# Optimization experiments

Hardware: AMD Instinct MI355X
Metric: run time of the kernel (lower is better)

## Reference

```python
import jax, jax.numpy as jnp
import numpy as np

EPS = 1e-5

def _gcn_norm(edge_index, num_nodes):
    # add self loops (improved=False -> fill value 1.0), symmetric normalization
    src = jnp.concatenate([edge_index[0], jnp.arange(num_nodes)])
    dst = jnp.concatenate([edge_index[1], jnp.arange(num_nodes)])
    w = jnp.ones(src.shape[0], dtype=jnp.float32)
    deg = jax.ops.segment_sum(w, dst, num_segments=num_nodes)
    dinv = jnp.where(deg > 0, 1.0 / jnp.sqrt(deg), 0.0)
    norm = dinv[src] * dinv[dst]  # [E+N]
    return src, dst, norm

def _gcn_conv(x, W, src, dst, norm, num_nodes):
    h = x @ W                      # [N, out]
    msg = h[src] * norm[:, None]   # gather + scale, [E+N, out]
    return jax.ops.segment_sum(msg, dst, num_segments=num_nodes)

def _bn_relu(x, gamma, beta):
    # BatchNorm1d in training mode: biased batch stats over the node dim
    m = x.mean(axis=0)
    v = x.var(axis=0)
    return jax.nn.relu((x - m) * jax.lax.rsqrt(v + EPS) * gamma + beta)

def setup_inputs() -> dict:
    key = jax.random.key(0)
    ks = jax.random.split(key, 12)
    N, E, D_IN, H, D_OUT, DEPTH = 100000, 1600000, 3, 128, 1, 9
    x = jax.random.normal(ks[0], (N, D_IN), dtype=jnp.float32)
    edge_index = jax.random.randint(ks[1], (2, E), 0, N, dtype=jnp.int64)
    s = 1.0 / np.sqrt(H)
    W0 = jax.random.normal(ks[2], (D_IN, H), jnp.float32) / np.sqrt(D_IN)
    Ws1 = jax.random.normal(ks[3], (DEPTH, H, H), jnp.float32) * s
    g1 = jnp.ones((DEPTH + 1, H), jnp.float32)
    b1 = jnp.zeros((DEPTH + 1, H), jnp.float32)
    Ws2 = jax.random.normal(ks[4], (DEPTH - 1, H, H), jnp.float32) * s
    g2 = jnp.ones((DEPTH - 1, H), jnp.float32)
    b2 = jnp.zeros((DEPTH - 1, H), jnp.float32)
    Wout = jax.random.normal(ks[5], (H, D_OUT), jnp.float32) * s
    return {"x": x, "edge_index": edge_index, "W0": W0, "Ws1": Ws1, "g1": g1,
            "b1": b1, "Ws2": Ws2, "g2": g2, "b2": b2, "Wout": Wout}

def reference(x, edge_index, W0, Ws1, g1, b1, Ws2, g2, b2, Wout):
    N = x.shape[0]
    depth = Ws1.shape[0]  # 9
    src, dst, norm = _gcn_norm(edge_index, N)
    # conv1[0]
    h = _bn_relu(_gcn_conv(x, W0, src, dst, norm, N), g1[0], b1[0])
    xs = [h]
    for i in range(1, depth + 1):
        h = _bn_relu(_gcn_conv(h, Ws1[i - 1], src, dst, norm, N), g1[i], b1[i])
        if i < depth:
            xs.append(h)
    for i in range(depth):
        j = depth - i - 1
        h = h + xs[j]
        if i < depth - 1:
            h = _bn_relu(_gcn_conv(h, Ws2[i], src, dst, norm, N), g2[i], b2[i])
        else:
            h = jax.nn.sigmoid(_gcn_conv(h, Wout, src, dst, norm, N))
    return h
```

## Files before the change

kernel.cpp:

```cpp
#include <hip/hip_runtime.h>
#include <hip/hip_bf16.h>

#define EPSV 1e-5f
#define NSTRIPE 16

typedef unsigned int uint;
typedef unsigned short ushort;
typedef __attribute__((ext_vector_type(8))) __bf16 bf16x8;
typedef __attribute__((ext_vector_type(4))) float f32x4;

static __device__ __forceinline__ float bf2f(ushort u) {
    return __uint_as_float(((uint)u) << 16);
}
static __device__ __forceinline__ ushort f2bf(float f) {
    __hip_bfloat16 h = __float2bfloat16(f);
    return __builtin_bit_cast(ushort, h);
}


static __device__ __forceinline__ float e4m3_dec(unsigned char b) {
    int s = b >> 7, E = (b >> 3) & 15, m = b & 7;
    float v = (E == 0) ? (float)m * 0.001953125f
                       : (float)(8 + m) * 0.125f * exp2f((float)(E - 7));
    return s ? -v : v;
}
static __device__ __forceinline__ unsigned char e4m3_enc(float f) {
    unsigned su = (__float_as_uint(f) >> 24) & 0x80u;
    float a = fabsf(f);
    if (!(a < 448.f)) return (unsigned char)(su | 0x7E);
    if (a < 0.015625f) {
        int m = (int)rintf(a * 512.f);
        return (unsigned char)(su | (m >= 8 ? 0x08 : m));
    }
    int e;
    frexpf(a, &e);
    int E = e - 1 + 7;
    float mant = a * exp2f((float)(1 - e)) - 1.0f;
    int mi = (int)rintf(mant * 8.f);
    if (mi >= 8) { mi = 0; E++; }
    if (E >= 16) return (unsigned char)(su | 0x7E);
    if (E == 15 && mi == 7) mi = 6;
    return (unsigned char)(su | (E << 3) | mi);
}


template <typename T> struct IOV;
template <> struct IOV<float> {
    static __device__ __forceinline__ float2 ld2(const float* p) { return *(const float2*)p; }
    static __device__ __forceinline__ void st2(float* p, float a, float b) {
        *(float2*)p = make_float2(a, b);
    }
    static __device__ __forceinline__ void ld8(const float* p, float* v) {
        float4 a = ((const float4*)p)[0], b = ((const float4*)p)[1];
        v[0] = a.x; v[1] = a.y; v[2] = a.z; v[3] = a.w;
        v[4] = b.x; v[5] = b.y; v[6] = b.z; v[7] = b.w;
    }
    static __device__ __forceinline__ void st8(float* p, const float* v) {
        ((float4*)p)[0] = make_float4(v[0], v[1], v[2], v[3]);
        ((float4*)p)[1] = make_float4(v[4], v[5], v[6], v[7]);
    }
};
template <> struct IOV<ushort> {
    static __device__ __forceinline__ float2 ld2(const ushort* p) {
        uint u = *(const uint*)p;
        return make_float2(bf2f((ushort)u), bf2f((ushort)(u >> 16)));
    }
    static __device__ __forceinline__ void st2(ushort* p, float a, float b) {
        *(uint*)p = (uint)f2bf(a) | ((uint)f2bf(b) << 16);
    }
    static __device__ __forceinline__ void ld8(const ushort* p, float* v) {
        uint4 u = *(const uint4*)p;
        v[0] = bf2f((ushort)u.x); v[1] = bf2f((ushort)(u.x >> 16));
        v[2] = bf2f((ushort)u.y); v[3] = bf2f((ushort)(u.y >> 16));
        v[4] = bf2f((ushort)u.z); v[5] = bf2f((ushort)(u.z >> 16));
        v[6] = bf2f((ushort)u.w); v[7] = bf2f((ushort)(u.w >> 16));
    }
    static __device__ __forceinline__ void st8(ushort* p, const float* v) {
        uint4 u;
        u.x = (uint)f2bf(v[0]) | ((uint)f2bf(v[1]) << 16);
        u.y = (uint)f2bf(v[2]) | ((uint)f2bf(v[3]) << 16);
        u.z = (uint)f2bf(v[4]) | ((uint)f2bf(v[5]) << 16);
        u.w = (uint)f2bf(v[6]) | ((uint)f2bf(v[7]) << 16);
        *(uint4*)p = u;
    }
};
template <> struct IOV<unsigned char> {
    static __device__ __forceinline__ float2 ld2(const unsigned char* p) {
        ushort u = *(const ushort*)p;
        return make_float2(e4m3_dec((unsigned char)u), e4m3_dec((unsigned char)(u >> 8)));
    }
    static __device__ __forceinline__ void st2(unsigned char* p, float a, float b) {
        *(ushort*)p = (ushort)e4m3_enc(a) | ((ushort)e4m3_enc(b) << 8);
    }
    static __device__ __forceinline__ void ld8(const unsigned char* p, float* v) {
        uint2 u = *(const uint2*)p;
#pragma unroll
        for (int j = 0; j < 4; j++) v[j] = e4m3_dec((unsigned char)(u.x >> (8 * j)));
#pragma unroll
        for (int j = 0; j < 4; j++) v[4 + j] = e4m3_dec((unsigned char)(u.y >> (8 * j)));
    }
    static __device__ __forceinline__ void st8(unsigned char* p, const float* v) {
        uint2 u = {0, 0};
#pragma unroll
        for (int j = 0; j < 4; j++) u.x |= (uint)e4m3_enc(v[j]) << (8 * j);
#pragma unroll
        for (int j = 0; j < 4; j++) u.y |= (uint)e4m3_enc(v[4 + j]) << (8 * j);
        *(uint2*)p = u;
    }
};


__global__ void k_count(const int* __restrict__ dst, int* __restrict__ cnt, int E) {
    int e = blockIdx.x * blockDim.x + threadIdx.x;
    if (e < E) atomicAdd(&cnt[dst[e]], 1);
}

__global__ void k_scan1(const int* __restrict__ cnt, int* __restrict__ bsum, int N) {
    __shared__ int s[256];
    int i = blockIdx.x * 256 + threadIdx.x;
    s[threadIdx.x] = (i < N) ? ((cnt[i] + 15) & ~15) : 0;
    __syncthreads();
    for (int o = 128; o > 0; o >>= 1) {
        if (threadIdx.x < o) s[threadIdx.x] += s[threadIdx.x + o];
        __syncthreads();
    }
    if (threadIdx.x == 0) bsum[blockIdx.x] = s[0];
}

__global__ void k_scan2(int* __restrict__ bsum, int B) {
    __shared__ int s[1024];
    int t = threadIdx.x;
    int orig = (t < B) ? bsum[t] : 0;
    s[t] = orig;
    __syncthreads();
    for (int o = 1; o < 1024; o <<= 1) {
        int v = (t >= o) ? s[t - o] : 0;
        __syncthreads();
        s[t] += v;
        __syncthreads();
    }
    if (t < B) bsum[t] = s[t] - orig;
}

__global__ void k_scan3(const int* __restrict__ cnt, const int* __restrict__ bsum,
                        int* __restrict__ roff, int* __restrict__ cursor,
                        float* __restrict__ dinv, int N) {
    __shared__ int s[256];
    int i = blockIdx.x * 256 + threadIdx.x;
    int v = (i < N) ? cnt[i] : 0;
    int pv = (v + 15) & ~15;
    s[threadIdx.x] = pv;
    __syncthreads();
    for (int o = 1; o < 256; o <<= 1) {
        int u = (threadIdx.x >= o) ? s[threadIdx.x - o] : 0;
        __syncthreads();
        s[threadIdx.x] += u;
        __syncthreads();
    }
    if (i < N) {
        int off = bsum[blockIdx.x] + s[threadIdx.x] - pv;
        roff[i] = off;
        cursor[i] = off;
        dinv[i] = rsqrtf((float)(v + 1));
        if (i == N - 1) roff[N] = off + pv;
    }
}

__global__ void k_scatter(const int* __restrict__ src, const int* __restrict__ dst,
                          const float* __restrict__ dinv, int* __restrict__ cursor,
                          int2* __restrict__ ev, int E) {
    int e = blockIdx.x * blockDim.x + threadIdx.x;
    if (e < E) {
        int s = src[e], d = dst[e];
        int p = atomicAdd(&cursor[d], 1);
        int2 pk;
        pk.x = s;
        pk.y = __float_as_int(dinv[s] * dinv[d]);
        ev[p] = pk;
    }
}

__global__ void k_pad(const int* __restrict__ cursor, const int* __restrict__ roff,
                      int2* __restrict__ ev, int N) {
    int i = blockIdx.x * blockDim.x + threadIdx.x;
    if (i >= N) return;
    int p = cursor[i], e = roff[i + 1];
    int2 pk;
    pk.x = i;
    pk.y = 0;
    for (; p < e; p++) ev[p] = pk;
}

__global__ void k_prepw(const float* __restrict__ Ws1, const float* __restrict__ Ws2,
                        ushort* __restrict__ whi, ushort* __restrict__ wlo) {
    int idx = blockIdx.x * blockDim.x + threadIdx.x;
    if (idx >= 17 * 16384) return;
    int L = idx >> 14, r = idx & 16383;
    int f = r >> 9, e = r & 511, lane = e >> 3, j = e & 7;
    int n = (f >> 2) * 16 + (lane & 15);
    int k = (f & 3) * 32 + (lane >> 4) * 8 + j;
    const float* W = (L < 9) ? (Ws1 + (size_t)L * 16384) : (Ws2 + (size_t)(L - 9) * 16384);
    float w = W[(size_t)k * 128 + n];
    ushort hi = f2bf(w);
    whi[idx] = hi;
    wlo[idx] = f2bf(w - bf2f(hi));
}


__global__ void k_spmm3(const float* __restrict__ X, const int2* __restrict__ ev,
                        const int* __restrict__ roff, const float* __restrict__ dinv,
                        float* __restrict__ XA, int N) {
    int i = blockIdx.x * blockDim.x + threadIdx.x;
    if (i >= N) return;
    float di = dinv[i];
    float w0 = di * di;
    float a0 = X[(size_t)i * 3 + 0] * w0;
    float a1 = X[(size_t)i * 3 + 1] * w0;
    float a2 = X[(size_t)i * 3 + 2] * w0;
    int je = roff[i + 1];
    for (int j = roff[i]; j < je; j++) {
        int2 e = ev[j];
        float w = __int_as_float(e.y);
        a0 += X[(size_t)e.x * 3 + 0] * w;
        a1 += X[(size_t)e.x * 3 + 1] * w;
        a2 += X[(size_t)e.x * 3 + 2] * w;
    }
    XA[(size_t)i * 3 + 0] = a0;
    XA[(size_t)i * 3 + 1] = a1;
    XA[(size_t)i * 3 + 2] = a2;
}

template <typename ZT>
__global__ __launch_bounds__(256) void k_spmm_stats(
    const ushort* __restrict__ H, const int2* __restrict__ ev,
    const int* __restrict__ roff, const float* __restrict__ dinv,
    ZT* __restrict__ Y, float* __restrict__ st, int N) {
    int lane = threadIdx.x & 63, wv = threadIdx.x >> 6;
    int i = blockIdx.x * 4 + wv;
    const uint* Hu = (const uint*)H;
    float a0 = 0.f, a1 = 0.f;

    if (i < N) {
        float di = dinv[i];
        float ws = di * di;
        uint u = Hu[(size_t)i * 64 + lane];
        a0 = bf2f((ushort)u) * ws;
        a1 = bf2f((ushort)(u >> 16)) * ws;
        int j = roff[i], je = roff[i + 1];
        for (; j < je; j += 16) {
            int2 e[16];
            uint uu[16];
#pragma unroll
            for (int t = 0; t < 16; t++) e[t] = ev[j + t];
#pragma unroll
            for (int t = 0; t < 16; t++) uu[t] = Hu[(size_t)e[t].x * 64 + lane];
#pragma unroll
            for (int t = 0; t < 16; t++) {
                float w = __int_as_float(e[t].y);
                a0 += bf2f((ushort)uu[t]) * w;
                a1 += bf2f((ushort)(uu[t] >> 16)) * w;
            }
        }
        IOV<ZT>::st2(&Y[(size_t)i * 128 + 2 * lane], a0, a1);
    }

    __shared__ float ls[4][64][4];
    ls[wv][lane][0] = a0; ls[wv][lane][1] = a1;
    ls[wv][lane][2] = a0 * a0; ls[wv][lane][3] = a1 * a1;
    __syncthreads();
    if (wv == 0) {
        float s0 = ls[0][lane][0] + ls[1][lane][0] + ls[2][lane][0] + ls[3][lane][0];
        float s1 = ls[0][lane][1] + ls[1][lane][1] + ls[2][lane][1] + ls[3][lane][1];
        float q0 = ls[0][lane][2] + ls[1][lane][2] + ls[2][lane][2] + ls[3][lane][2];
        float q1 = ls[0][lane][3] + ls[1][lane][3] + ls[2][lane][3] + ls[3][lane][3];
        float* stp = st + (size_t)(blockIdx.x & (NSTRIPE - 1)) * 256;
        atomicAdd(&stp[2 * lane], s0);
        atomicAdd(&stp[2 * lane + 1], s1);
        atomicAdd(&stp[128 + 2 * lane], q0);
        atomicAdd(&stp[129 + 2 * lane], q1);
    }
}

__global__ void k_spmm1(const float* __restrict__ T, const int2* __restrict__ ev,
                        const int* __restrict__ roff, const float* __restrict__ dinv,
                        float* __restrict__ out, int N) {
    int i = blockIdx.x * blockDim.x + threadIdx.x;
    if (i >= N) return;
    float di = dinv[i];
    float a = T[i] * di * di;
    int je = roff[i + 1];
    for (int j = roff[i]; j < je; j++) {
        int2 e = ev[j];
        a += T[e.x] * __int_as_float(e.y);
    }
    out[i] = 1.0f / (1.0f + expf(-a));
}

__global__ void k_bnfin(const float* __restrict__ st, const float* __restrict__ g,
                        const float* __restrict__ b, float* __restrict__ aff, float invN) {
    int c = threadIdx.x;
    float S = 0.f, Q = 0.f;
    for (int s = 0; s < NSTRIPE; s++) {
        S += st[(size_t)s * 256 + c];
        Q += st[(size_t)s * 256 + 128 + c];
    }
    float m = S * invN;
    float var = Q * invN - m * m;
    float sc = g[c] * rsqrtf(var + EPSV);
    aff[c] = sc;
    aff[128 + c] = b[c] - m * sc;
}


template <typename ZT>
__global__ __launch_bounds__(256) void k_gemm3_stats(
    const float* __restrict__ XA, const float* __restrict__ W0,
    ZT* __restrict__ Y, float* __restrict__ st, int N) {
    int lane = threadIdx.x & 63, wv = threadIdx.x >> 6;
    int i = blockIdx.x * 4 + wv;
    float y0 = 0.f, y1 = 0.f;
    if (i < N) {
        int c0 = lane * 2;
        float x0 = XA[(size_t)i * 3], x1 = XA[(size_t)i * 3 + 1], x2 = XA[(size_t)i * 3 + 2];
        y0 = x0 * W0[c0] + x1 * W0[128 + c0] + x2 * W0[256 + c0];
        y1 = x0 * W0[c0 + 1] + x1 * W0[128 + c0 + 1] + x2 * W0[256 + c0 + 1];
        IOV<ZT>::st2(&Y[(size_t)i * 128 + c0], y0, y1);
    }
    __shared__ float ls[4][64][4];
    ls[wv][lane][0] = y0; ls[wv][lane][1] = y1;
    ls[wv][lane][2] = y0 * y0; ls[wv][lane][3] = y1 * y1;
    __syncthreads();
    if (wv == 0) {
        float s0 = ls[0][lane][0] + ls[1][lane][0] + ls[2][lane][0] + ls[3][lane][0];
        float s1 = ls[0][lane][1] + ls[1][lane][1] + ls[2][lane][1] + ls[3][lane][1];
        float q0 = ls[0][lane][2] + ls[1][lane][2] + ls[2][lane][2] + ls[3][lane][2];
        float q1 = ls[0][lane][3] + ls[1][lane][3] + ls[2][lane][3] + ls[3][lane][3];
        float* stp = st + (size_t)(blockIdx.x & (NSTRIPE - 1)) * 256;
        atomicAdd(&stp[2 * lane], s0);
        atomicAdd(&stp[2 * lane + 1], s1);
        atomicAdd(&stp[128 + 2 * lane], q0);
        atomicAdd(&stp[129 + 2 * lane], q1);
    }
}

template <typename ZT, typename SKT>
__global__ __launch_bounds__(256) void k_gemm_mfma(
    const ZT* __restrict__ Z, const SKT* __restrict__ skip_in, SKT* __restrict__ skip_out,
    const float* __restrict__ st, const float* __restrict__ gz, const float* __restrict__ bz,
    const ushort* __restrict__ whi, const ushort* __restrict__ wlo,
    ushort* __restrict__ H, float invN, int N) {
    __shared__ ushort sW[16384];
    __shared__ float sA[256];
    int tid = threadIdx.x;
    int wave = tid >> 6, lane = tid & 63;
    int l15 = lane & 15, quad = lane >> 4;

    {
        float acc = 0.f;
#pragma unroll
        for (int s = 0; s < NSTRIPE; s++) acc += st[(size_t)s * 256 + tid];
        sA[tid] = acc;
    }
    {
        const uint4* src = (const uint4*)whi;
#pragma unroll
        for (int t = 0; t < 8; t++) ((uint4*)sW)[tid + 256 * t] = src[tid + 256 * t];
    }
    __syncthreads();
    if (tid < 128) {
        float S = sA[tid], Q = sA[128 + tid];
        float m = S * invN;
        float var = Q * invN - m * m;
        float sc = gz[tid] * rsqrtf(var + EPSV);
        sA[tid] = sc;
        sA[128 + tid] = bz[tid] - m * sc;
    }
    __syncthreads();

    int row = blockIdx.x * 64 + wave * 16 + l15;
    size_t rowc = (size_t)(row < N ? row : N - 1);

    bf16x8 ahi[4];
#pragma unroll
    for (int kc = 0; kc < 4; kc++) {
        int c0 = kc * 32 + quad * 8;
        float v[8];
        IOV<ZT>::ld8(&Z[rowc * 128 + c0], v);
        float av[8];
#pragma unroll
        for (int jj = 0; jj < 8; jj++) {
            float t = v[jj] * sA[c0 + jj] + sA[128 + c0 + jj];
            av[jj] = fmaxf(t, 0.f);
        }
        if (skip_out && row < N) IOV<SKT>::st8(&skip_out[rowc * 128 + c0], av);
        if (skip_in) {
            float w2[8];
            IOV<SKT>::ld8(&skip_in[rowc * 128 + c0], w2);
#pragma unroll
            for (int jj = 0; jj < 8; jj++) av[jj] += w2[jj];
        }
        bf16x8 fh;
#pragma unroll
        for (int jj = 0; jj < 8; jj++) fh[jj] = (__bf16)av[jj];
        ahi[kc] = fh;
    }

    f32x4 acc[8];
#pragma unroll
    for (int ct = 0; ct < 8; ct++) {
        f32x4 z0 = {0.f, 0.f, 0.f, 0.f};
        acc[ct] = z0;
    }

#pragma unroll
    for (int ct = 0; ct < 8; ct++) {
#pragma unroll
        for (int kc = 0; kc < 4; kc++) {
            bf16x8 b = *(const bf16x8*)&sW[(ct * 4 + kc) * 512 + lane * 8];
            acc[ct] = __builtin_amdgcn_mfma_f32_16x16x32_bf16(ahi[kc], b, acc[ct], 0, 0, 0);
        }
    }
    __syncthreads();
    {
        const uint4* src = (const uint4*)wlo;
#pragma unroll
        for (int t = 0; t < 8; t++) ((uint4*)sW)[tid + 256 * t] = src[tid + 256 * t];
    }
    __syncthreads();
#pragma unroll
    for (int ct = 0; ct < 8; ct++) {
#pragma unroll
        for (int kc = 0; kc < 4; kc++) {
            bf16x8 b = *(const bf16x8*)&sW[(ct * 4 + kc) * 512 + lane * 8];
            acc[ct] = __builtin_amdgcn_mfma_f32_16x16x32_bf16(ahi[kc], b, acc[ct], 0, 0, 0);
        }
    }
    __syncthreads();
    ushort* sC = sW;
#pragma unroll
    for (int ct = 0; ct < 8; ct++)
#pragma unroll
        for (int reg = 0; reg < 4; reg++) {
            int r = wave * 16 + quad * 4 + reg;
            sC[r * 136 + ct * 16 + l15] = f2bf(acc[ct][reg]);
        }
    __syncthreads();
    for (int t = tid; t < 1024; t += 256) {
        int r = t >> 4, c4 = t & 15;
        int grow = blockIdx.x * 64 + r;
        if (grow < N)
            ((uint4*)(H + (size_t)grow * 128))[c4] = *(const uint4*)&sC[r * 136 + c4 * 8];
    }
}

template <typename ZT, typename SKT>
__global__ __launch_bounds__(256) void k_dot(
    const ZT* __restrict__ Z, const SKT* __restrict__ S0,
    const float* __restrict__ aff, const float* __restrict__ Wout,
    float* __restrict__ T, int N) {
    int i = blockIdx.x * 4 + (threadIdx.x >> 6);
    if (i >= N) return;
    int lane = threadIdx.x & 63;
    int c0 = 2 * lane, c1 = c0 + 1;
    float2 z = IOV<ZT>::ld2(&Z[(size_t)i * 128 + c0]);
    float2 s = IOV<SKT>::ld2(&S0[(size_t)i * 128 + c0]);
    float p0 = fmaxf(z.x * aff[c0] + aff[128 + c0], 0.f) + s.x;
    float p1 = fmaxf(z.y * aff[c1] + aff[128 + c1], 0.f) + s.y;
    float a = p0 * Wout[c0] + p1 * Wout[c1];
    for (int o = 32; o > 0; o >>= 1) a += __shfl_down(a, o);
    if (lane == 0) T[i] = a;
}


template <typename ZT, typename SKT>
static void run_all(const float* x, const int* src, const int* dst, const float* W0,
                    const float* Ws1, const float* g1, const float* b1,
                    const float* Ws2, const float* g2, const float* b2,
                    const float* Wout, float* out, char* ws, int N, int E,
                    hipStream_t stream) {
    char* p = ws;
    auto alloc = [&](size_t bytes) -> void* {
        void* r = (void*)p;
        p += (bytes + 255) & ~(size_t)255;
        return r;
    };
    size_t Epad = (size_t)E + 15 * (size_t)N + 16;
    int*   roff   = (int*)alloc((size_t)(N + 1) * 4);
    float* dinv   = (float*)alloc((size_t)N * 4);
    int2*  ev     = (int2*)alloc(Epad * 8);
    int*   bsum   = (int*)alloc(4096);
    float* st_all = (float*)alloc((size_t)18 * NSTRIPE * 256 * 4);
    float* aff    = (float*)alloc(1024);
    ushort* whi   = (ushort*)alloc((size_t)17 * 16384 * 2);
    ushort* wlo   = (ushort*)alloc((size_t)17 * 16384 * 2);
    size_t nz = (size_t)N * 128;
    ushort* hb = (ushort*)alloc(nz * 2);
    ZT* zb = (ZT*)alloc(nz * sizeof(ZT));
    SKT* skips = (SKT*)alloc((size_t)9 * nz * sizeof(SKT));
    auto skip = [&](int s) { return skips + (size_t)s * nz; };
    auto stg  = [&](int s) { return st_all + (size_t)s * NSTRIPE * 256; };

    int* cnt    = (int*)skip(8);
    int* cursor = (int*)((char*)skip(8) + (((size_t)N * 4 + 255) & ~(size_t)255));
    float* xa   = (float*)hb;
    float* tbuf = (float*)hb;

    float invN = 1.0f / (float)N;
    auto gb = [&](int stage, const float** g, const float** b) {
        if (stage <= 9) { *g = g1 + (size_t)stage * 128; *b = b1 + (size_t)stage * 128; }
        else { *g = g2 + (size_t)(stage - 10) * 128; *b = b2 + (size_t)(stage - 10) * 128; }
    };

    hipMemsetAsync(st_all, 0, (size_t)18 * NSTRIPE * 256 * 4, stream);
    hipMemsetAsync(cnt, 0, (size_t)N * 4, stream);
    k_count<<<(E + 255) / 256, 256, 0, stream>>>(dst, cnt, E);
    int B = (N + 255) / 256;
    k_scan1<<<B, 256, 0, stream>>>(cnt, bsum, N);
    k_scan2<<<1, 1024, 0, stream>>>(bsum, B);
    k_scan3<<<B, 256, 0, stream>>>(cnt, bsum, roff, cursor, dinv, N);
    k_scatter<<<(E + 255) / 256, 256, 0, stream>>>(src, dst, dinv, cursor, ev, E);
    k_pad<<<(N + 255) / 256, 256, 0, stream>>>(cursor, roff, ev, N);
    k_prepw<<<(17 * 16384 + 255) / 256, 256, 0, stream>>>(Ws1, Ws2, whi, wlo);

    int gg = (N + 63) / 64;
    int gs4 = (N + 3) / 4;

    k_spmm3<<<(N + 255) / 256, 256, 0, stream>>>(x, ev, roff, dinv, xa, N);
    k_gemm3_stats<ZT><<<gs4, 256, 0, stream>>>(xa, W0, zb, stg(0), N);

    for (int l = 1; l <= 9; l++) {
        const float *gzp, *bzp;
        gb(l - 1, &gzp, &bzp);
        k_gemm_mfma<ZT, SKT><<<gg, 256, 0, stream>>>(
            zb, (const SKT*)nullptr, skip(l - 1), stg(l - 1), gzp, bzp,
            whi + (size_t)(l - 1) * 16384, wlo + (size_t)(l - 1) * 16384, hb, invN, N);
        k_spmm_stats<ZT><<<gs4, 256, 0, stream>>>(hb, ev, roff, dinv, zb, stg(l), N);
    }

    for (int i = 0; i < 8; i++) {
        int zs = 9 + i;
        const float *gzp, *bzp;
        gb(zs, &gzp, &bzp);
        k_gemm_mfma<ZT, SKT><<<gg, 256, 0, stream>>>(
            zb, skip(8 - i), (SKT*)nullptr, stg(zs), gzp, bzp,
            whi + (size_t)(9 + i) * 16384, wlo + (size_t)(9 + i) * 16384, hb, invN, N);
        k_spmm_stats<ZT><<<gs4, 256, 0, stream>>>(hb, ev, roff, dinv, zb, stg(10 + i), N);
    }

    const float *gzp, *bzp;
    gb(17, &gzp, &bzp);
    k_bnfin<<<1, 128, 0, stream>>>(stg(17), gzp, bzp, aff, invN);
    k_dot<ZT, SKT><<<gs4, 256, 0, stream>>>(zb, skip(0), aff, Wout, tbuf, N);
    k_spmm1<<<(N + 255) / 256, 256, 0, stream>>>(tbuf, ev, roff, dinv, out, N);
}


extern "C" void kernel_launch(void* const* d_in, const int* in_sizes, int n_in,
                              void* d_out, int out_size, void* d_ws, size_t ws_size,
                              hipStream_t stream) {
    const float* x    = (const float*)d_in[0];
    const int*   ei   = (const int*)d_in[1];
    const float* W0   = (const float*)d_in[2];
    const float* Ws1  = (const float*)d_in[3];
    const float* g1   = (const float*)d_in[4];
    const float* b1   = (const float*)d_in[5];
    const float* Ws2  = (const float*)d_in[6];
    const float* g2   = (const float*)d_in[7];
    const float* b2   = (const float*)d_in[8];
    const float* Wout = (const float*)d_in[9];
    float* out = (float*)d_out;

    int N = in_sizes[0] / 3;
    int E = in_sizes[1] / 2;
    const int* src = ei;
    const int* dst = ei + E;

    size_t nz = (size_t)N * 128;
    size_t Epad = (size_t)E + 15 * (size_t)N + 16;
    auto need = [&](size_t zbytes, size_t skbytes) -> size_t {
        size_t t = 0;
        auto add = [&](size_t b) { t += (b + 255) & ~(size_t)255; };
        add((size_t)(N + 1) * 4);
        add((size_t)N * 4);
        add(Epad * 8);
        add(4096);
        add((size_t)18 * NSTRIPE * 256 * 4);
        add(1024);
        add((size_t)17 * 16384 * 2);
        add((size_t)17 * 16384 * 2);
        add(nz * 2);
        add(nz * zbytes);
        add((size_t)9 * nz * skbytes);
        return t;
    };

    char* ws = (char*)d_ws;
    if (need(4, 2) <= ws_size)
        run_all<float, ushort>(x, src, dst, W0, Ws1, g1, b1, Ws2, g2, b2, Wout, out, ws, N, E, stream);
    else if (need(4, 1) <= ws_size)
        run_all<float, unsigned char>(x, src, dst, W0, Ws1, g1, b1, Ws2, g2, b2, Wout, out, ws, N, E, stream);
    else
        run_all<ushort, unsigned char>(x, src, dst, W0, Ws1, g1, b1, Ws2, g2, b2, Wout, out, ws, N, E, stream);
}
```

Before: 2.412 ms.

## Factor GCN normalization into row scaling and store edges as bare indices

Rewrites the symmetric normalization D^-1/2 A D^-1/2 so the source-side dinv is folded into the GEMM epilogue and the destination-side dinv is applied after aggregation. Edge records shrink from int2 (index plus weight) to a single int, and padding entries now point at a zero row N that the GEMM writes. This halves edge-list traffic in the hot SpMM loop and drops a multiply per neighbour. The cost is an extra zero row in the hidden buffer, one more GEMM block, and a separate count array.

```diff
diff --git a/kernel.cpp b/kernel.cpp
--- a/kernel.cpp
+++ b/kernel.cpp
@@ -167,28 +167,20 @@
 }
 
 __global__ void k_scatter(const int* __restrict__ src, const int* __restrict__ dst,
-                          const float* __restrict__ dinv, int* __restrict__ cursor,
-                          int2* __restrict__ ev, int E) {
+                          int* __restrict__ cursor, int* __restrict__ ev, int E) {
     int e = blockIdx.x * blockDim.x + threadIdx.x;
     if (e < E) {
-        int s = src[e], d = dst[e];
-        int p = atomicAdd(&cursor[d], 1);
-        int2 pk;
-        pk.x = s;
-        pk.y = __float_as_int(dinv[s] * dinv[d]);
-        ev[p] = pk;
+        int p = atomicAdd(&cursor[dst[e]], 1);
+        ev[p] = src[e];
     }
 }
 
 __global__ void k_pad(const int* __restrict__ cursor, const int* __restrict__ roff,
-                      int2* __restrict__ ev, int N) {
+                      int* __restrict__ ev, int N) {
     int i = blockIdx.x * blockDim.x + threadIdx.x;
     if (i >= N) return;
     int p = cursor[i], e = roff[i + 1];
-    int2 pk;
-    pk.x = i;
-    pk.y = 0;
-    for (; p < e; p++) ev[p] = pk;
+    for (; p < e; p++) ev[p] = N;
 }
 
 __global__ void k_prepw(const float* __restrict__ Ws1, const float* __restrict__ Ws2,
@@ -207,32 +199,31 @@
 }
 
 
-__global__ void k_spmm3(const float* __restrict__ X, const int2* __restrict__ ev,
-                        const int* __restrict__ roff, const float* __restrict__ dinv,
-                        float* __restrict__ XA, int N) {
+__global__ void k_spmm3(const float* __restrict__ X, const int* __restrict__ ev,
+                        const int* __restrict__ cnt, const int* __restrict__ roff,
+                        const float* __restrict__ dinv, float* __restrict__ XA, int N) {
     int i = blockIdx.x * blockDim.x + threadIdx.x;
     if (i >= N) return;
     float di = dinv[i];
-    float w0 = di * di;
-    float a0 = X[(size_t)i * 3 + 0] * w0;
-    float a1 = X[(size_t)i * 3 + 1] * w0;
-    float a2 = X[(size_t)i * 3 + 2] * w0;
-    int je = roff[i + 1];
-    for (int j = roff[i]; j < je; j++) {
-        int2 e = ev[j];
-        float w = __int_as_float(e.y);
-        a0 += X[(size_t)e.x * 3 + 0] * w;
-        a1 += X[(size_t)e.x * 3 + 1] * w;
-        a2 += X[(size_t)e.x * 3 + 2] * w;
-    }
-    XA[(size_t)i * 3 + 0] = a0;
-    XA[(size_t)i * 3 + 1] = a1;
-    XA[(size_t)i * 3 + 2] = a2;
+    float a0 = X[(size_t)i * 3 + 0] * di;
+    float a1 = X[(size_t)i * 3 + 1] * di;
+    float a2 = X[(size_t)i * 3 + 2] * di;
+    int jb = roff[i], je = jb + cnt[i];
+    for (int j = jb; j < je; j++) {
+        int s = ev[j];
+        float ds = dinv[s];
+        a0 += X[(size_t)s * 3 + 0] * ds;
+        a1 += X[(size_t)s * 3 + 1] * ds;
+        a2 += X[(size_t)s * 3 + 2] * ds;
+    }
+    XA[(size_t)i * 3 + 0] = a0 * di;
+    XA[(size_t)i * 3 + 1] = a1 * di;
+    XA[(size_t)i * 3 + 2] = a2 * di;
 }
 
 template <typename ZT>
 __global__ __launch_bounds__(256) void k_spmm_stats(
-    const ushort* __restrict__ H, const int2* __restrict__ ev,
+    const ushort* __restrict__ H, const int* __restrict__ ev,
     const int* __restrict__ roff, const float* __restrict__ dinv,
     ZT* __restrict__ Y, float* __restrict__ st, int N) {
     int lane = threadIdx.x & 63, wv = threadIdx.x >> 6;
@@ -241,26 +232,26 @@
     float a0 = 0.f, a1 = 0.f;
 
     if (i < N) {
-        float di = dinv[i];
-        float ws = di * di;
         uint u = Hu[(size_t)i * 64 + lane];
-        a0 = bf2f((ushort)u) * ws;
-        a1 = bf2f((ushort)(u >> 16)) * ws;
+        a0 = bf2f((ushort)u);
+        a1 = bf2f((ushort)(u >> 16));
         int j = roff[i], je = roff[i + 1];
         for (; j < je; j += 16) {
-            int2 e[16];
+            int e[16];
             uint uu[16];
 #pragma unroll
             for (int t = 0; t < 16; t++) e[t] = ev[j + t];
 #pragma unroll
-            for (int t = 0; t < 16; t++) uu[t] = Hu[(size_t)e[t].x * 64 + lane];
+            for (int t = 0; t < 16; t++) uu[t] = Hu[(size_t)e[t] * 64 + lane];
 #pragma unroll
             for (int t = 0; t < 16; t++) {
-                float w = __int_as_float(e[t].y);
-                a0 += bf2f((ushort)uu[t]) * w;
-                a1 += bf2f((ushort)(uu[t] >> 16)) * w;
+                a0 += bf2f((ushort)uu[t]);
+                a1 += bf2f((ushort)(uu[t] >> 16));
             }
         }
+        float di = dinv[i];
+        a0 *= di;
+        a1 *= di;
         IOV<ZT>::st2(&Y[(size_t)i * 128 + 2 * lane], a0, a1);
     }
 
@@ -281,18 +272,19 @@
     }
 }
 
-__global__ void k_spmm1(const float* __restrict__ T, const int2* __restrict__ ev,
-                        const int* __restrict__ roff, const float* __restrict__ dinv,
-                        float* __restrict__ out, int N) {
+__global__ void k_spmm1(const float* __restrict__ T, const int* __restrict__ ev,
+                        const int* __restrict__ cnt, const int* __restrict__ roff,
+                        const float* __restrict__ dinv, float* __restrict__ out, int N) {
     int i = blockIdx.x * blockDim.x + threadIdx.x;
     if (i >= N) return;
     float di = dinv[i];
-    float a = T[i] * di * di;
-    int je = roff[i + 1];
-    for (int j = roff[i]; j < je; j++) {
-        int2 e = ev[j];
-        a += T[e.x] * __int_as_float(e.y);
-    }
+    float a = T[i] * di;
+    int jb = roff[i], je = jb + cnt[i];
+    for (int j = jb; j < je; j++) {
+        int s = ev[j];
+        a += T[s] * dinv[s];
+    }
+    a *= di;
     out[i] = 1.0f / (1.0f + expf(-a));
 }
 
@@ -348,18 +340,24 @@
     const ZT* __restrict__ Z, const SKT* __restrict__ skip_in, SKT* __restrict__ skip_out,
     const float* __restrict__ st, const float* __restrict__ gz, const float* __restrict__ bz,
     const ushort* __restrict__ whi, const ushort* __restrict__ wlo,
-    ushort* __restrict__ H, float invN, int N) {
+    const float* __restrict__ dinv, ushort* __restrict__ H, float invN, int N) {
     __shared__ ushort sW[16384];
     __shared__ float sA[256];
+    __shared__ float sD[64];
     int tid = threadIdx.x;
     int wave = tid >> 6, lane = tid & 63;
     int l15 = lane & 15, quad = lane >> 4;
+    int row0 = blockIdx.x * 64;
 
     {
         float acc = 0.f;
 #pragma unroll
         for (int s = 0; s < NSTRIPE; s++) acc += st[(size_t)s * 256 + tid];
         sA[tid] = acc;
+    }
+    if (tid < 64) {
+        int r = row0 + tid;
+        sD[tid] = (r < N) ? dinv[r] : 0.f;
     }
     {
         const uint4* src = (const uint4*)whi;
@@ -377,7 +375,7 @@
     }
     __syncthreads();
 
-    int row = blockIdx.x * 64 + wave * 16 + l15;
+    int row = row0 + wave * 16 + l15;
     size_t rowc = (size_t)(row < N ? row : N - 1);
 
     bf16x8 ahi[4];
@@ -442,14 +440,16 @@
 #pragma unroll
         for (int reg = 0; reg < 4; reg++) {
             int r = wave * 16 + quad * 4 + reg;
-            sC[r * 136 + ct * 16 + l15] = f2bf(acc[ct][reg]);
+            sC[r * 136 + ct * 16 + l15] = f2bf(acc[ct][reg] * sD[r]);
         }
     __syncthreads();
     for (int t = tid; t < 1024; t += 256) {
         int r = t >> 4, c4 = t & 15;
-        int grow = blockIdx.x * 64 + r;
+        int grow = row0 + r;
         if (grow < N)
             ((uint4*)(H + (size_t)grow * 128))[c4] = *(const uint4*)&sC[r * 136 + c4 * 8];
+        else if (grow == N)
+            ((uint4*)(H + (size_t)grow * 128))[c4] = make_uint4(0, 0, 0, 0);
     }
 }
 
@@ -487,21 +487,21 @@
     size_t Epad = (size_t)E + 15 * (size_t)N + 16;
     int*   roff   = (int*)alloc((size_t)(N + 1) * 4);
     float* dinv   = (float*)alloc((size_t)N * 4);
-    int2*  ev     = (int2*)alloc(Epad * 8);
+    int*   cnt    = (int*)alloc((size_t)N * 4);
+    int*   ev     = (int*)alloc(Epad * 4);
     int*   bsum   = (int*)alloc(4096);
     float* st_all = (float*)alloc((size_t)18 * NSTRIPE * 256 * 4);
     float* aff    = (float*)alloc(1024);
     ushort* whi   = (ushort*)alloc((size_t)17 * 16384 * 2);
     ushort* wlo   = (ushort*)alloc((size_t)17 * 16384 * 2);
     size_t nz = (size_t)N * 128;
-    ushort* hb = (ushort*)alloc(nz * 2);
+    ushort* hb = (ushort*)alloc((nz + 128) * 2);
     ZT* zb = (ZT*)alloc(nz * sizeof(ZT));
     SKT* skips = (SKT*)alloc((size_t)9 * nz * sizeof(SKT));
     auto skip = [&](int s) { return skips + (size_t)s * nz; };
     auto stg  = [&](int s) { return st_all + (size_t)s * NSTRIPE * 256; };
 
-    int* cnt    = (int*)skip(8);
-    int* cursor = (int*)((char*)skip(8) + (((size_t)N * 4 + 255) & ~(size_t)255));
+    int* cursor = (int*)skip(8);
     float* xa   = (float*)hb;
     float* tbuf = (float*)hb;
 
@@ -518,14 +518,14 @@
     k_scan1<<<B, 256, 0, stream>>>(cnt, bsum, N);
     k_scan2<<<1, 1024, 0, stream>>>(bsum, B);
     k_scan3<<<B, 256, 0, stream>>>(cnt, bsum, roff, cursor, dinv, N);
-    k_scatter<<<(E + 255) / 256, 256, 0, stream>>>(src, dst, dinv, cursor, ev, E);
+    k_scatter<<<(E + 255) / 256, 256, 0, stream>>>(src, dst, cursor, ev, E);
     k_pad<<<(N + 255) / 256, 256, 0, stream>>>(cursor, roff, ev, N);
     k_prepw<<<(17 * 16384 + 255) / 256, 256, 0, stream>>>(Ws1, Ws2, whi, wlo);
 
-    int gg = (N + 63) / 64;
+    int gg = (N + 64) / 64;
     int gs4 = (N + 3) / 4;
 
-    k_spmm3<<<(N + 255) / 256, 256, 0, stream>>>(x, ev, roff, dinv, xa, N);
+    k_spmm3<<<(N + 255) / 256, 256, 0, stream>>>(x, ev, cnt, roff, dinv, xa, N);
     k_gemm3_stats<ZT><<<gs4, 256, 0, stream>>>(xa, W0, zb, stg(0), N);
 
     for (int l = 1; l <= 9; l++) {
@@ -533,7 +533,7 @@
         gb(l - 1, &gzp, &bzp);
         k_gemm_mfma<ZT, SKT><<<gg, 256, 0, stream>>>(
             zb, (const SKT*)nullptr, skip(l - 1), stg(l - 1), gzp, bzp,
-            whi + (size_t)(l - 1) * 16384, wlo + (size_t)(l - 1) * 16384, hb, invN, N);
+            whi + (size_t)(l - 1) * 16384, wlo + (size_t)(l - 1) * 16384, dinv, hb, invN, N);
         k_spmm_stats<ZT><<<gs4, 256, 0, stream>>>(hb, ev, roff, dinv, zb, stg(l), N);
     }
 
@@ -543,7 +543,7 @@
         gb(zs, &gzp, &bzp);
         k_gemm_mfma<ZT, SKT><<<gg, 256, 0, stream>>>(
             zb, skip(8 - i), (SKT*)nullptr, stg(zs), gzp, bzp,
-            whi + (size_t)(9 + i) * 16384, wlo + (size_t)(9 + i) * 16384, hb, invN, N);
+            whi + (size_t)(9 + i) * 16384, wlo + (size_t)(9 + i) * 16384, dinv, hb, invN, N);
         k_spmm_stats<ZT><<<gs4, 256, 0, stream>>>(hb, ev, roff, dinv, zb, stg(10 + i), N);
     }
 
@@ -551,7 +551,7 @@
     gb(17, &gzp, &bzp);
     k_bnfin<<<1, 128, 0, stream>>>(stg(17), gzp, bzp, aff, invN);
     k_dot<ZT, SKT><<<gs4, 256, 0, stream>>>(zb, skip(0), aff, Wout, tbuf, N);
-    k_spmm1<<<(N + 255) / 256, 256, 0, stream>>>(tbuf, ev, roff, dinv, out, N);
+    k_spmm1<<<(N + 255) / 256, 256, 0, stream>>>(tbuf, ev, cnt, roff, dinv, out, N);
 }
 
 
@@ -582,13 +582,14 @@
         auto add = [&](size_t b) { t += (b + 255) & ~(size_t)255; };
         add((size_t)(N + 1) * 4);
         add((size_t)N * 4);
-        add(Epad * 8);
+        add((size_t)N * 4);
+        add(Epad * 4);
         add(4096);
         add((size_t)18 * NSTRIPE * 256 * 4);
         add(1024);
         add((size_t)17 * 16384 * 2);
         add((size_t)17 * 16384 * 2);
-        add(nz * 2);
+        add((nz + 128) * 2);
         add(nz * zbytes);
         add((size_t)9 * nz * skbytes);
         return t;
```

New measurement: 2.538 ms. +5.2%, slower.
